# Performance work log

Hardware: AMD Instinct MI355X
Metric: run time of the kernel (lower is better)

The kernel has to match this reference:

```python
import jax, jax.numpy as jnp
import numpy as np

VOXEL = 64        # voxel_size from init_kwargs
SHARPNESS = 100.0 # sigmoid sharpness in original forward
EPS = 1e-8


def make_coords(V):
    # Grid of (x, y) points in [0,1]^2, row-major over (y, x) like torch.meshgrid 'ij'.
    y, x = jnp.meshgrid(jnp.arange(V), jnp.arange(V), indexing='ij')
    coords = jnp.stack([x.ravel(), y.ravel()], axis=1).astype(jnp.float32)
    return coords / np.float32(V - 1)  # [M, 2], M = V*V


def setup_inputs() -> dict:
    key = jax.random.key(0)
    k1, k2, k3 = jax.random.split(key, 3)
    B, N, P = 8, 32, 32
    # Vertices uniform in [0,1)^2: all rows sum != 0, so the original's per-vertex
    # validity mask keeps every vertex (P >= 3), matching this static-shape reference.
    polygons = jax.random.uniform(k1, (B, N, P, 2), dtype=jnp.float32)
    attributes = jax.random.uniform(k2, (B, 4), dtype=jnp.float32)
    validity_scores = jax.random.uniform(k3, (B, N), dtype=jnp.float32)
    return {"polygons": polygons, "attributes": attributes, "validity_scores": validity_scores}


def _polygon_sdf(polygons, coords):
    # polygons: [B, N, P, 2]; coords: [M, 2] -> sdf [B, N, M]
    v0 = polygons[:, :, :, None, :]                         # [B,N,P,1,2]
    v1 = jnp.roll(polygons, shift=-1, axis=2)[:, :, :, None, :]
    pts = coords[None, None, None, :, :]                    # [1,1,1,M,2]
    e = v1 - v0                                             # edge vectors
    v = pts - v0                                            # point - vertex
    e_norm_sq = (e * e).sum(-1, keepdims=True) + EPS
    t = jnp.clip((v * e).sum(-1, keepdims=True) / e_norm_sq, 0.0, 1.0)
    diff = v - t * e                                        # pts - projection
    dists = jnp.sqrt((diff * diff).sum(-1))                 # [B,N,P,M]
    min_dist = dists.min(axis=2)                            # [B,N,M]

    # Crossing-number inside test
    x_pts = coords[None, None, None, :, 0]                  # [1,1,1,M]
    y_pts = coords[None, None, None, :, 1]
    x0, y0 = v0[..., 0], v0[..., 1]                         # [B,N,P,1]
    x1, y1 = v1[..., 0], v1[..., 1]
    y_crosses = ((y0 <= y_pts) & (y1 > y_pts)) | ((y1 <= y_pts) & (y0 > y_pts))
    inter_x = x0 + (x1 - x0) * ((y_pts - y0) / (y1 - y0 + EPS))
    crossings = (inter_x > x_pts) & y_crosses               # [B,N,P,M]
    inside = (crossings.sum(axis=2) % 2) == 1               # [B,N,M]
    return jnp.where(inside, -min_dist, min_dist)


def reference(polygons, attributes, validity_scores):
    B, N, P, _ = polygons.shape
    V = VOXEL
    coords = make_coords(V)                                 # [M,2]
    sdf = _polygon_sdf(polygons, coords)                    # [B,N,M]

    valid = validity_scores >= 0.5                          # [B,N]
    sdf = jnp.where(valid[:, :, None], sdf, 1.0)            # invalid polys -> sdf = 1
    masks = jax.nn.sigmoid(-sdf * SHARPNESS)                # [B,N,M]
    # Combined max only over valid polygons (invalid contribute 0, like the zero-init max loop)
    combined = jnp.where(valid[:, :, None], masks, 0.0).max(axis=1)  # [B,M]
    combined = combined.reshape(B, V, V)                    # [B,H,W]

    # height_voxels = clamp(int(attr0 * D), 1, D)
    h = jnp.clip(jnp.floor(attributes[:, 0] * V).astype(jnp.int32), 1, V)  # [B]
    depth_mask = (jnp.arange(V)[None, :] < h[:, None]).astype(combined.dtype)  # [B,D]
    voxels = depth_mask[:, :, None, None] * combined[:, None, :, :]  # [B,D,H,W]
    return voxels
```

## Files before the change

kernel.cpp:

```cpp
#include <hip/hip_runtime.h>
#include <math.h>

#define VOX 64
#define NPOLY 32
#define NEDGE 32
#define NET (NPOLY * NEDGE)

__global__ __launch_bounds__(512, 2) void extrusion_kernel(
    const float* __restrict__ polygons,
    const float* __restrict__ attributes,
    const float* __restrict__ validity,
    float* __restrict__ out)
{
    __shared__ float4 ecA[NET];
    __shared__ float4 ecB[NET];
    __shared__ float  partial[8][VOX];
    __shared__ float  comb[VOX];
    __shared__ int    vIdx[NPOLY];
    __shared__ int    nValidS;

    const int t   = threadIdx.x;
    const int b   = blockIdx.x >> 6;
    const int row = blockIdx.x & 63;
    const float py = (float)row * (1.0f / 63.0f);

    if (t < 64) {
        bool f = (t < NPOLY) && (validity[b * NPOLY + t] >= 0.5f);
        unsigned long long m = __ballot(f);
        if (f) vIdx[__popcll(m & ((1ull << t) - 1ull))] = t;
        if (t == 0) nValidS = (int)__popcll(m);
    }

    const float2* pb = (const float2*)(polygons + (size_t)b * NET * 2);
    for (int e = t; e < NET; e += 512) {
        int n  = e >> 5;
        int k  = e & 31;
        int k1 = (k + 1) & 31;
        float2 v0 = pb[n * NEDGE + k];
        float2 v1 = pb[n * NEDGE + k1];
        float ex = v1.x - v0.x;
        float ey = v1.y - v0.y;
        float inv = 1.0f / (ex * ex + ey * ey + 1e-8f);
        float vy  = py - v0.y;
        float c1  = vy * ey;
        bool ycross = ((v0.y <= py) && (v1.y > py)) || ((v1.y <= py) && (v0.y > py));
        float ix = ycross ? (v0.x + ex * (vy / (ey + 1e-8f))) : -1e30f;
        ecA[e] = make_float4(v0.x, ex, ey, inv);
        ecB[e] = make_float4(c1, vy, ix, 0.0f);
    }
    __syncthreads();

    const int g  = t >> 6;
    const int lx = t & 63;
    const float px = (float)lx * (1.0f / 63.0f);
    const int nV = nValidS;
    float minsdf = 1e30f;
    for (int j = g; j < nV; j += 8) {
        int base = vIdx[j] * NEDGE;
        float mind2 = 1e30f;
        int cnt = 0;
        #pragma unroll
        for (int k = 0; k < NEDGE; ++k) {
            float4 A  = ecA[base + k];
            float4 Bc = ecB[base + k];
            float vx  = px - A.x;
            float dot = fmaf(vx, A.y, Bc.x);
            float tt  = fminf(fmaxf(dot * A.w, 0.0f), 1.0f);
            float dx  = fmaf(-tt, A.y, vx);
            float dy  = fmaf(-tt, A.z, Bc.y);
            float d2  = fmaf(dy, dy, dx * dx);
            mind2 = fminf(mind2, d2);
            cnt += (Bc.z > px) ? 1 : 0;
        }
        float d = sqrtf(mind2);
        minsdf = fminf(minsdf, (cnt & 1) ? -d : d);
    }
    partial[g][lx] = minsdf;
    __syncthreads();

    if (t < VOX) {
        float m = partial[0][t];
        #pragma unroll
        for (int gg = 1; gg < 8; ++gg) m = fminf(m, partial[gg][t]);
        comb[t] = 1.0f / (1.0f + __expf(100.0f * m));
    }
    __syncthreads();

    float att = attributes[b * 4 + 0];
    int h = max(1, min(64, (int)floorf(att * 64.0f)));

    float4* out4 = (float4*)out;
    const int q  = t & 15;
    const int z0 = t >> 4;
    float4 cv = make_float4(comb[q * 4 + 0], comb[q * 4 + 1],
                            comb[q * 4 + 2], comb[q * 4 + 3]);
    float4 zero = make_float4(0.f, 0.f, 0.f, 0.f);
    size_t base4 = (size_t)b * 65536 + (size_t)row * 16 + q;
    out4[base4 + (size_t)z0 * 1024]        = (z0 < h)        ? cv : zero;
    out4[base4 + (size_t)(z0 + 32) * 1024] = ((z0 + 32) < h) ? cv : zero;
}

extern "C" void kernel_launch(void* const* d_in, const int* in_sizes, int n_in,
                              void* d_out, int out_size, void* d_ws, size_t ws_size,
                              hipStream_t stream) {
    const float* polygons   = (const float*)d_in[0];
    const float* attributes = (const float*)d_in[1];
    const float* validity   = (const float*)d_in[2];
    float* out = (float*)d_out;
    const int B = in_sizes[2] / NPOLY;
    dim3 grid(B * VOX);
    dim3 block(512);
    extrusion_kernel<<<grid, block, 0, stream>>>(polygons, attributes, validity, out);
}
```

Before: 70.21 us.

## Map wave lanes to polygon edges and reduce per pixel with DPP

The per-thread distance loop is remapped so that each lane owns one polygon edge and iterates over 32 pixels, instead of owning one pixel and iterating over 32 edges. The per-pixel minimum squared distance is reduced across each 32-lane half with DPP row shifts and readlane. Crossing parity comes from a ballot plus popcount. This removes the per-edge LDS loads from the inner loop, but adds about a dozen cross-lane operations per pixel step. The signed minimum is kept in squared form and square-rooted once at the end.

```diff
diff --git a/kernel.cpp b/kernel.cpp
--- a/kernel.cpp
+++ b/kernel.cpp
@@ -5,6 +5,13 @@
 #define NPOLY 32
 #define NEDGE 32
 #define NET (NPOLY * NEDGE)
+
+template<int CTRL>
+__device__ __forceinline__ float dppmin(float x) {
+    int s = __builtin_amdgcn_update_dpp(0x7f800000, __float_as_int(x),
+                                        CTRL, 0xF, 0xF, false);
+    return fminf(x, __int_as_float(s));
+}
 
 __global__ __launch_bounds__(512, 2) void extrusion_kernel(
     const float* __restrict__ polygons,
@@ -51,31 +58,48 @@
     __syncthreads();
 
     const int g  = t >> 6;
-    const int lx = t & 63;
-    const float px = (float)lx * (1.0f / 63.0f);
+    const int l  = t & 63;
+    const int ke = l & 31;
+    const float hx = (float)(l >> 5) * (1.0f / 63.0f);
+    const int halfp = l >> 1;
+    const int lodd  = l & 1;
     const int nV = nValidS;
-    float minsdf = 1e30f;
+
+    float acc = 1e36f;
     for (int j = g; j < nV; j += 8) {
-        int base = vIdx[j] * NEDGE;
-        float mind2 = 1e30f;
-        int cnt = 0;
-        #pragma unroll
-        for (int k = 0; k < NEDGE; ++k) {
-            float4 A  = ecA[base + k];
-            float4 Bc = ecB[base + k];
+        const int e0 = vIdx[j] * NEDGE + ke;
+        const float4 A  = ecA[e0];
+        const float4 Bc = ecB[e0];
+        #pragma unroll 8
+        for (int p = 0; p < 32; ++p) {
+            float px  = fmaf((float)p, 2.0f / 63.0f, hx);
             float vx  = px - A.x;
-            float dot = fmaf(vx, A.y, Bc.x);
-            float tt  = fminf(fmaxf(dot * A.w, 0.0f), 1.0f);
+            float w   = fmaf(vx, A.y, Bc.x);
+            float tt  = fminf(fmaxf(w * A.w, 0.0f), 1.0f);
             float dx  = fmaf(-tt, A.y, vx);
             float dy  = fmaf(-tt, A.z, Bc.y);
             float d2  = fmaf(dy, dy, dx * dx);
-            mind2 = fminf(mind2, d2);
-            cnt += (Bc.z > px) ? 1 : 0;
+            float m = d2;
+            m = dppmin<0x111>(m);
+            m = dppmin<0x112>(m);
+            m = dppmin<0x114>(m);
+            m = dppmin<0x118>(m);
+            m = dppmin<0x142>(m);
+            float m0 = __int_as_float(__builtin_amdgcn_readlane(__float_as_int(m), 31));
+            float m1 = __int_as_float(__builtin_amdgcn_readlane(__float_as_int(m), 63));
+            unsigned long long cm = __ballot(Bc.z > px);
+            int par0 = ((int)__popcll(cm & 0xffffffffull)) & 1;
+            int par1 = ((int)__popcll(cm >> 32)) & 1;
+            float k0 = par0 ? -m0 : m0;
+            float k1 = par1 ? -m1 : m1;
+            float kk = lodd ? k1 : k0;
+            acc = (halfp == p) ? fminf(acc, kk) : acc;
         }
-        float d = sqrtf(mind2);
-        minsdf = fminf(minsdf, (cnt & 1) ? -d : d);
     }
-    partial[g][lx] = minsdf;
+    {
+        float ad = sqrtf(fabsf(acc));
+        partial[g][l] = (acc < 0.0f) ? -ad : ad;
+    }
     __syncthreads();
 
     if (t < VOX) {
```

Result: slower. 79.38 us (+13.1%).

## Double block size to 1024 threads and split edge loop into independent min chains

Applied to the files above, without the earlier changes.

Raises the block to 1024 threads so each thread precomputes exactly one edge, 16 polygon groups share the per-row work, and each thread writes one output depth slice. The inner edge loop processes two edges per iteration with four independent min accumulators to expose instruction-level parallelism. The sqrt is deferred to once per thread by min-reducing signed squared distances. The launch bound of 1024 threads with min 8 blocks may force heavy register limits and spilling. Fewer blocks fit per CU, and the larger block raises synchronisation cost.

```diff
diff --git a/kernel.cpp b/kernel.cpp
--- a/kernel.cpp
+++ b/kernel.cpp
@@ -6,7 +6,7 @@
 #define NEDGE 32
 #define NET (NPOLY * NEDGE)
 
-__global__ __launch_bounds__(512, 2) void extrusion_kernel(
+__global__ __launch_bounds__(1024, 8) void extrusion_kernel(
     const float* __restrict__ polygons,
     const float* __restrict__ attributes,
     const float* __restrict__ validity,
@@ -14,7 +14,7 @@
 {
     __shared__ float4 ecA[NET];
     __shared__ float4 ecB[NET];
-    __shared__ float  partial[8][VOX];
+    __shared__ float  partial[16][VOX];
     __shared__ float  comb[VOX];
     __shared__ int    vIdx[NPOLY];
     __shared__ int    nValidS;
@@ -32,10 +32,11 @@
     }
 
     const float2* pb = (const float2*)(polygons + (size_t)b * NET * 2);
-    for (int e = t; e < NET; e += 512) {
-        int n  = e >> 5;
-        int k  = e & 31;
-        int k1 = (k + 1) & 31;
+    {
+        const int e  = t;
+        const int n  = e >> 5;
+        const int k  = e & 31;
+        const int k1 = (k + 1) & 31;
         float2 v0 = pb[n * NEDGE + k];
         float2 v1 = pb[n * NEDGE + k1];
         float ex = v1.x - v0.x;
@@ -54,34 +55,53 @@
     const int lx = t & 63;
     const float px = (float)lx * (1.0f / 63.0f);
     const int nV = nValidS;
-    float minsdf = 1e30f;
-    for (int j = g; j < nV; j += 8) {
-        int base = vIdx[j] * NEDGE;
-        float mind2 = 1e30f;
-        int cnt = 0;
-        #pragma unroll
-        for (int k = 0; k < NEDGE; ++k) {
-            float4 A  = ecA[base + k];
-            float4 Bc = ecB[base + k];
-            float vx  = px - A.x;
-            float dot = fmaf(vx, A.y, Bc.x);
-            float tt  = fminf(fmaxf(dot * A.w, 0.0f), 1.0f);
-            float dx  = fmaf(-tt, A.y, vx);
-            float dy  = fmaf(-tt, A.z, Bc.y);
-            float d2  = fmaf(dy, dy, dx * dx);
-            mind2 = fminf(mind2, d2);
-            cnt += (Bc.z > px) ? 1 : 0;
+
+    float acc = 1e36f;
+    for (int j = g; j < nV; j += 16) {
+        const int base = vIdx[j] * NEDGE;
+        float mv0 = 1e30f, mv1 = 1e30f, mv2 = 1e30f, mv3 = 1e30f;
+        int   c0 = 0, c1n = 0;
+        #pragma unroll 4
+        for (int k = 0; k < NEDGE; k += 2) {
+            float4 A0  = ecA[base + k];
+            float4 B0  = ecB[base + k];
+            float4 A1  = ecA[base + k + 1];
+            float4 B1  = ecB[base + k + 1];
+
+            float vx0  = px - A0.x;
+            float dot0 = fmaf(vx0, A0.y, B0.x);
+            float tt0  = fminf(fmaxf(dot0 * A0.w, 0.0f), 1.0f);
+            float dx0  = fmaf(-tt0, A0.y, vx0);
+            float dy0  = fmaf(-tt0, A0.z, B0.y);
+            float d20  = fmaf(dy0, dy0, dx0 * dx0);
+
+            float vx1  = px - A1.x;
+            float dot1 = fmaf(vx1, A1.y, B1.x);
+            float tt1  = fminf(fmaxf(dot1 * A1.w, 0.0f), 1.0f);
+            float dx1  = fmaf(-tt1, A1.y, vx1);
+            float dy1  = fmaf(-tt1, A1.z, B1.y);
+            float d21  = fmaf(dy1, dy1, dx1 * dx1);
+
+            if ((k & 2) == 0) { mv0 = fminf(mv0, d20); mv1 = fminf(mv1, d21); }
+            else              { mv2 = fminf(mv2, d20); mv3 = fminf(mv3, d21); }
+            c0  += (B0.z > px) ? 1 : 0;
+            c1n += (B1.z > px) ? 1 : 0;
         }
-        float d = sqrtf(mind2);
-        minsdf = fminf(minsdf, (cnt & 1) ? -d : d);
+        float mind2 = fminf(fminf(mv0, mv1), fminf(mv2, mv3));
+        int cnt = c0 + c1n;
+        float key = (cnt & 1) ? -mind2 : mind2;
+        acc = fminf(acc, key);
     }
-    partial[g][lx] = minsdf;
+    {
+        float ad = sqrtf(fabsf(acc));
+        partial[g][lx] = (acc < 0.0f) ? -ad : ad;
+    }
     __syncthreads();
 
     if (t < VOX) {
         float m = partial[0][t];
         #pragma unroll
-        for (int gg = 1; gg < 8; ++gg) m = fminf(m, partial[gg][t]);
+        for (int gg = 1; gg < 16; ++gg) m = fminf(m, partial[gg][t]);
         comb[t] = 1.0f / (1.0f + __expf(100.0f * m));
     }
     __syncthreads();
@@ -90,14 +110,13 @@
     int h = max(1, min(64, (int)floorf(att * 64.0f)));
 
     float4* out4 = (float4*)out;
-    const int q  = t & 15;
-    const int z0 = t >> 4;
+    const int q = t & 15;
+    const int z = t >> 4;
     float4 cv = make_float4(comb[q * 4 + 0], comb[q * 4 + 1],
                             comb[q * 4 + 2], comb[q * 4 + 3]);
     float4 zero = make_float4(0.f, 0.f, 0.f, 0.f);
     size_t base4 = (size_t)b * 65536 + (size_t)row * 16 + q;
-    out4[base4 + (size_t)z0 * 1024]        = (z0 < h)        ? cv : zero;
-    out4[base4 + (size_t)(z0 + 32) * 1024] = ((z0 + 32) < h) ? cv : zero;
+    out4[base4 + (size_t)z * 1024] = (z < h) ? cv : zero;
 }
 
 extern "C" void kernel_launch(void* const* d_in, const int* in_sizes, int n_in,
@@ -109,6 +128,6 @@
     float* out = (float*)d_out;
     const int B = in_sizes[2] / NPOLY;
     dim3 grid(B * VOX);
-    dim3 block(512);
+    dim3 block(1024);
     extrusion_kernel<<<grid, block, 0, stream>>>(polygons, attributes, validity, out);
 }
```

After: 69.83 us. About the same (-0.5%).
